# Kernel optimization log

Measured on AMD Instinct MI355X. Metric: run time of the kernel, lower is better.

The kernel has to match this reference:

```python
import jax, jax.numpy as jnp
import numpy as np
import math

B, S, CIN, H, W = 8, 8, 64, 32, 32
COUT, K = 128, 3
PW = COUT * CIN * K * K  # 73728
P = PW + COUT            # 73856


def setup_inputs() -> dict:
    key = jax.random.key(0)
    ks = jax.random.split(key, 6)
    return {
        "x": jax.random.normal(ks[0], (B, S, CIN, H, W), dtype=jnp.float32),
        "e": jax.random.normal(ks[1], (S, P), dtype=jnp.float32),
        "mu_w": jax.random.normal(ks[2], (PW,), dtype=jnp.float32) * 0.02,
        "rho_w": jax.random.normal(ks[3], (PW,), dtype=jnp.float32) * 0.5,
        "mu_b": jax.random.normal(ks[4], (COUT,), dtype=jnp.float32) * 0.02,
        "rho_b": jax.random.normal(ks[5], (COUT,), dtype=jnp.float32) * 0.5,
    }


def _unit_log_mfg(v):
    # v: [s_n, D]; -log(2*pi)*D/2 - sum(v**2)/2  (scalar, matching torch code)
    two_pi = jnp.asarray(2.0 * math.pi, v.dtype)
    return -jnp.log(two_pi) * (v.shape[1] / 2.0) - jnp.sum(v * v) / 2.0


def reference(x, e, mu_w, rho_w, mu_b, rho_b):
    s_n = e.shape[0]
    cout = mu_b.shape[0]
    cin = x.shape[2]
    k = int(round(math.sqrt(mu_w.shape[0] / (cout * cin))))
    pw = mu_w.shape[0]

    sig_w = jax.nn.softplus(rho_w)  # log(1+exp(rho))
    sig_b = jax.nn.softplus(rho_b)
    w = mu_w[None, :] + sig_w[None, :] * e[:, :pw]          # [s_n, PW]
    b = mu_b[None, :] + sig_b[None, :] * e[:, pw:pw + cout]  # [s_n, COUT]

    entropy_q = jnp.sum(jnp.log(sig_w)) + jnp.sum(jnp.log(sig_b))
    cross_entropy_qp = _unit_log_mfg(w) + _unit_log_mfg(b)
    kl_qp = -entropy_q - cross_entropy_qp

    w5 = w.reshape(s_n, cout, cin, k, k)  # per-sample OIHW kernels

    # per-sample conv: vmap over the sample axis j; batch conv over data axis i
    def conv_one(xj, wj):  # xj [B,CIN,H,W], wj [COUT,CIN,K,K]
        return jax.lax.conv(xj, wj, (1, 1), 'VALID')

    out = jax.vmap(conv_one, in_axes=(1, 0), out_axes=1)(x, w5)  # [B,S,COUT,H',W']
    out = out + b[None, :, :, None, None]
    return out, kl_qp
```

## Files before the change

kernel.cpp:

```cpp
#include <hip/hip_runtime.h>
#include <hip/hip_bf16.h>
#include <math.h>

#define Bn    8
#define Sn    8
#define COUTc 128
#define PWc   73728
#define Pc    73856
#define WOc   30
#define NPIX  900
#define GPIX  7200
#define NSTEP 9
#define TILE  128
#define NT2   57
#define NSLOT 129

typedef __bf16 bf16;
typedef bf16  bf16x8 __attribute__((ext_vector_type(8)));
typedef float f32x4v __attribute__((ext_vector_type(4)));
typedef float f32x16 __attribute__((ext_vector_type(16)));

__device__ __forceinline__ float softplus_f(float x) {
    return fmaxf(x, 0.f) + log1pf(expf(-fabsf(x)));
}

__device__ __forceinline__ unsigned int pack2(float a, float b) {
    unsigned short ua = __builtin_bit_cast(unsigned short, (bf16)a);
    unsigned short ub = __builtin_bit_cast(unsigned short, (bf16)b);
    return ((unsigned int)ub << 16) | (unsigned int)ua;
}

__device__ __forceinline__ void gl16(const void* g, void* l) {
    typedef __attribute__((address_space(1))) void gvoid;
    typedef __attribute__((address_space(3))) void lvoid;
    __builtin_amdgcn_global_load_lds((gvoid*)g, (lvoid*)l, 16, 0, 0);
}

__global__ __launch_bounds__(256) void prep_all(
        const float* __restrict__ xg, const float* __restrict__ e,
        const float* __restrict__ mu_w, const float* __restrict__ rho_w,
        const float* __restrict__ mu_b, const float* __restrict__ rho_b,
        bf16* __restrict__ xt, bf16* __restrict__ wimg,
        float* __restrict__ bq, float* __restrict__ slots) {
    const int bid = blockIdx.x;
    const int t   = threadIdx.x;

    if (bid < 512) {
        const int img = bid >> 3;
        const int oct = t & 7;
        const int p0  = ((bid & 7) * 32 + (t >> 3)) * 4;
        const float* src = xg + ((size_t)img << 16) + (size_t)(oct * 8) * 1024 + p0;
        f32x4v v[8];
        #pragma unroll
        for (int j = 0; j < 8; ++j)
            v[j] = *reinterpret_cast<const f32x4v*>(src + (size_t)j * 1024);
        char* dstB = (char*)xt + (((size_t)(img << 10) + p0) << 7) + (oct << 4);
        #pragma unroll
        for (int i = 0; i < 4; ++i) {
            uint4 pk;
            pk.x = pack2(v[0][i], v[1][i]);
            pk.y = pack2(v[2][i], v[3][i]);
            pk.z = pack2(v[4][i], v[5][i]);
            pk.w = pack2(v[6][i], v[7][i]);
            *reinterpret_cast<uint4*>(dstB + (size_t)i * 128) = pk;
        }
        return;
    }

    float ls = 0.f, sq = 0.f;
    if (bid < 640) {
        const int rb    = bid - 512;
        const int sg2   = rb >> 5;
        const int chunk = rb & 31;
        const int gidx  = chunk * 256 + t;
        const int co    = gidx >> 6;
        const int ci    = gidx & 63;
        const int p0    = co * 576 + ci * 9;
        float mu[9], sg[9];
        #pragma unroll
        for (int r = 0; r < 9; ++r) {
            mu[r] = mu_w[p0 + r];
            sg[r] = softplus_f(rho_w[p0 + r]);
        }
        if (sg2 == 0) {
            #pragma unroll
            for (int r = 0; r < 9; ++r) ls += logf(sg[r]);
        }
        const int dstp = (co << 6) + (((ci >> 3) ^ (co & 7)) << 3) + (ci & 7);
        #pragma unroll
        for (int si = 0; si < 2; ++si) {
            const int s = sg2 * 2 + si;
            const float* es = e + s * Pc + p0;
            #pragma unroll
            for (int r = 0; r < 9; ++r) {
                float wv = fmaf(sg[r], es[r], mu[r]);
                wimg[((s * NSTEP + r) << 13) + dstp] = (bf16)wv;
                sq += wv * wv;
            }
        }
    } else {
        if (t < COUTc) {
            float sig = softplus_f(rho_b[t]);
            ls = logf(sig);
            float mu = mu_b[t];
            #pragma unroll
            for (int s = 0; s < Sn; ++s) {
                float bv = fmaf(sig, e[s * Pc + PWc + t], mu);
                bq[s * COUTc + t] = bv;
                sq += bv * bv;
            }
        }
    }

    #pragma unroll
    for (int off = 32; off > 0; off >>= 1) {
        ls += __shfl_down(ls, off);
        sq += __shfl_down(sq, off);
    }
    __shared__ float sls[4], ssq[4];
    const int lane = t & 63, wd = t >> 6;
    if (lane == 0) { sls[wd] = ls; ssq[wd] = sq; }
    __syncthreads();
    if (t == 0) {
        slots[2 * (bid - 512)]     = sls[0] + sls[1] + sls[2] + sls[3];
        slots[2 * (bid - 512) + 1] = ssq[0] + ssq[1] + ssq[2] + ssq[3];
    }
}

__global__ __launch_bounds__(256) void conv_mfma(
        const bf16* __restrict__ xt, const bf16* __restrict__ wimg,
        const float* __restrict__ bq, const float* __restrict__ slots,
        float* __restrict__ out, float* __restrict__ klout) {
    const int bid  = blockIdx.x;
    const int s    = bid & 7;
    const int tile = bid >> 3;
    const int t    = threadIdx.x;
    const int lane = t & 63;
    const int w    = t >> 6;
    const int wr   = w >> 1;
    const int wc   = w & 1;

    __shared__ bf16 Wbuf[2][8192];
    __shared__ bf16 Xbuf[2][8192];

    const char* wsrcL = (const char*)wimg + ((size_t)(s * NSTEP) << 14)
                      + (w << 12) + (lane << 4);

    const char *x0, *x1, *x2, *x3;
    #pragma unroll
    for (int q = 0; q < 4; ++q) {
        int pix = w * 32 + q * 8 + (lane >> 3);
        int g   = tile * TILE + pix;
        if (g >= GPIX) g = GPIX - 1;
        int b2 = g / NPIX;
        int rr = g - b2 * NPIX;
        int oy = rr / WOc;
        int ox = rr - oy * WOc;
        int m  = (lane & 7) ^ (pix & 7);
        const char* ptr = (const char*)xt
            + ((((size_t)(b2 * Sn + s) << 10) + oy * 32 + ox) << 7) + (m << 4);
        if (q == 0) x0 = ptr; else if (q == 1) x1 = ptr;
        else if (q == 2) x2 = ptr; else x3 = ptr;
    }

    f32x16 acc[2][2];
    #pragma unroll
    for (int i = 0; i < 2; ++i)
        #pragma unroll
        for (int j = 0; j < 2; ++j)
            #pragma unroll
            for (int k = 0; k < 16; ++k)
                acc[i][j][k] = 0.f;

    #define STAGE(stepc, b)                                                  \
    {                                                                        \
        const char* ws_ = wsrcL + ((stepc) << 14);                           \
        char* wl_ = (char*)(&Wbuf[(b)][0]) + (w << 12);                      \
        gl16(ws_,        wl_);                                               \
        gl16(ws_ + 1024, wl_ + 1024);                                        \
        gl16(ws_ + 2048, wl_ + 2048);                                        \
        gl16(ws_ + 3072, wl_ + 3072);                                        \
        const int roff_ = (((stepc) / 3) * 32 + ((stepc) % 3)) * 128;        \
        char* xl_ = (char*)(&Xbuf[(b)][0]) + (w << 12);                      \
        gl16(x0 + roff_, xl_);                                               \
        gl16(x1 + roff_, xl_ + 1024);                                        \
        gl16(x2 + roff_, xl_ + 2048);                                        \
        gl16(x3 + roff_, xl_ + 3072);                                        \
    }

    #define COMPUTE(b)                                                       \
    {                                                                        \
        const bf16* Wl_ = &Wbuf[(b)][0];                                     \
        const bf16* Xl_ = &Xbuf[(b)][0];                                     \
        _Pragma("unroll")                                                    \
        for (int kc = 0; kc < 4; ++kc) {                                     \
            const int oct_ = ((kc << 1) + (lane >> 5)) ^ (lane & 7);         \
            bf16x8 af0 = *reinterpret_cast<const bf16x8*>(                   \
                Wl_ + ((wr * 64 + (lane & 31)) << 6) + (oct_ << 3));         \
            bf16x8 af1 = *reinterpret_cast<const bf16x8*>(                   \
                Wl_ + ((wr * 64 + 32 + (lane & 31)) << 6) + (oct_ << 3));    \
            bf16x8 bf0 = *reinterpret_cast<const bf16x8*>(                   \
                Xl_ + ((wc * 64 + (lane & 31)) << 6) + (oct_ << 3));         \
            bf16x8 bf1 = *reinterpret_cast<const bf16x8*>(                   \
                Xl_ + ((wc * 64 + 32 + (lane & 31)) << 6) + (oct_ << 3));    \
            acc[0][0] = __builtin_amdgcn_mfma_f32_32x32x16_bf16(af0, bf0, acc[0][0], 0, 0, 0); \
            acc[0][1] = __builtin_amdgcn_mfma_f32_32x32x16_bf16(af0, bf1, acc[0][1], 0, 0, 0); \
            acc[1][0] = __builtin_amdgcn_mfma_f32_32x32x16_bf16(af1, bf0, acc[1][0], 0, 0, 0); \
            acc[1][1] = __builtin_amdgcn_mfma_f32_32x32x16_bf16(af1, bf1, acc[1][1], 0, 0, 0); \
        }                                                                    \
    }

    STAGE(0, 0);
    STAGE(1, 1);

    #define ITER(tt, b)                                                      \
        asm volatile("s_waitcnt vmcnt(8)" ::: "memory");                     \
        __builtin_amdgcn_s_barrier();                                        \
        __builtin_amdgcn_sched_barrier(0);                                   \
        COMPUTE(b);                                                          \
        __builtin_amdgcn_sched_barrier(0);                                   \
        __builtin_amdgcn_s_barrier();                                        \
        STAGE((tt) + 2, b);

    ITER(0, 0)
    ITER(1, 1)
    ITER(2, 0)
    ITER(3, 1)
    ITER(4, 0)
    ITER(5, 1)
    ITER(6, 0)
    asm volatile("s_waitcnt vmcnt(8)" ::: "memory");
    __builtin_amdgcn_s_barrier();
    __builtin_amdgcn_sched_barrier(0);
    COMPUTE(1);
    asm volatile("s_waitcnt vmcnt(0)" ::: "memory");
    __builtin_amdgcn_s_barrier();
    __builtin_amdgcn_sched_barrier(0);
    COMPUTE(0);

    #undef ITER
    #undef COMPUTE
    #undef STAGE

    const int colp = lane & 31;
    const int hi   = lane >> 5;
    #pragma unroll
    for (int ti = 0; ti < 2; ++ti) {
        float bs[16];
        #pragma unroll
        for (int reg = 0; reg < 16; ++reg) {
            int co = wr * 64 + ti * 32 + (reg & 3) + 8 * (reg >> 2) + 4 * hi;
            bs[reg] = bq[s * COUTc + co];
        }
        #pragma unroll
        for (int tj = 0; tj < 2; ++tj) {
            int gg = tile * TILE + wc * 64 + tj * 32 + colp;
            if (gg >= GPIX) continue;
            int b2 = gg / NPIX;
            int r2 = gg - b2 * NPIX;
            float* ob = out + (size_t)(b2 * Sn + s) * (COUTc * NPIX) + r2;
            #pragma unroll
            for (int reg = 0; reg < 16; ++reg) {
                int co = wr * 64 + ti * 32 + (reg & 3) + 8 * (reg >> 2) + 4 * hi;
                ob[co * NPIX] = acc[ti][tj][reg] + bs[reg];
            }
        }
    }

    if (bid == 0 && w == 0) {
        float ls = 0.f, sq = 0.f;
        for (int i2 = lane; i2 < NSLOT; i2 += 64) {
            ls += slots[2 * i2];
            sq += slots[2 * i2 + 1];
        }
        #pragma unroll
        for (int off = 32; off > 0; off >>= 1) {
            ls += __shfl_down(ls, off);
            sq += __shfl_down(sq, off);
        }
        if (lane == 0)
            *klout = -ls + 0.91893853320467274f * (float)Pc + 0.5f * sq;
    }
}

extern "C" void kernel_launch(void* const* d_in, const int* in_sizes, int n_in,
                              void* d_out, int out_size, void* d_ws, size_t ws_size,
                              hipStream_t stream) {
    const float* x     = (const float*)d_in[0];
    const float* e     = (const float*)d_in[1];
    const float* mu_w  = (const float*)d_in[2];
    const float* rho_w = (const float*)d_in[3];
    const float* mu_b  = (const float*)d_in[4];
    const float* rho_b = (const float*)d_in[5];
    float* out = (float*)d_out;

    bf16*  wimg  = (bf16*)d_ws;
    float* bq    = (float*)((char*)d_ws + 1179648);
    float* slots = (float*)((char*)d_ws + 1183744);
    bf16*  xt    = (bf16*)((char*)d_ws + 1187840);

    prep_all<<<dim3(641), dim3(256), 0, stream>>>(
        x, e, mu_w, rho_w, mu_b, rho_b, xt, wimg, bq, slots);

    conv_mfma<<<dim3(NT2 * Sn), dim3(256), 0, stream>>>(
        xt, wimg, bq, slots, out, out + (out_size - 1));
}
```

Baseline: 30.85 us.

## Halve K-step size in conv MFMA pipeline to 18 half-steps with smaller LDS buffers

Splits each of the 9 filter-tap K-steps (64 channels) into two 32-channel half-steps, giving 18 pipeline stages. The LDS double buffers shrink from 32 KB to 16 KB and each stage issues 4 instead of 8 global-to-LDS loads, with a new XOR swizzle on 4 slots. The aim is to cut LDS use, which may let more blocks share a CU, and to use finer-grained prefetch. In exchange it doubles the barrier count and puts less MFMA work between each sync.

Result: slower. 32.09 us (+4.0%).

```diff
diff --git a/kernel.cpp b/kernel.cpp
--- a/kernel.cpp
+++ b/kernel.cpp
@@ -139,28 +139,39 @@
     const int w    = t >> 6;
     const int wr   = w >> 1;
     const int wc   = w & 1;
-
-    __shared__ bf16 Wbuf[2][8192];
-    __shared__ bf16 Xbuf[2][8192];
-
-    const char* wsrcL = (const char*)wimg + ((size_t)(s * NSTEP) << 14)
-                      + (w << 12) + (lane << 4);
-
-    const char *x0, *x1, *x2, *x3;
+    const int hi   = lane >> 5;
+    const int lo   = lane & 31;
+
+    __shared__ bf16 Wbuf[2][4096];
+    __shared__ bf16 Xbuf[2][4096];
+
+    const int srow  = lane >> 2;
+    const int sslot = lane & 3;
+    const int rb23  = (lane >> 4) & 3;
+
+    const char* wsp[2][2];
+    {
+        const int lowslot = sslot ^ rb23 ^ (srow & 3);
+        const char* base = (const char*)wimg + ((size_t)(s * NSTEP) << 14);
+        #pragma unroll
+        for (int q = 0; q < 2; ++q) {
+            int co = w * 32 + q * 16 + srow;
+            const char* p0 = base + co * 128 + lowslot * 16;
+            wsp[0][q] = p0 + (((lane >> 4) & 1) << 6);
+            wsp[1][q] = p0 + ((1 ^ ((lane >> 4) & 1)) << 6);
+        }
+    }
+
+    const char* xsp[2];
     #pragma unroll
-    for (int q = 0; q < 4; ++q) {
-        int pix = w * 32 + q * 8 + (lane >> 3);
+    for (int q = 0; q < 2; ++q) {
+        int pix = w * 32 + q * 16 + srow;
         int g   = tile * TILE + pix;
         if (g >= GPIX) g = GPIX - 1;
-        int b2 = g / NPIX;
-        int rr = g - b2 * NPIX;
-        int oy = rr / WOc;
-        int ox = rr - oy * WOc;
-        int m  = (lane & 7) ^ (pix & 7);
-        const char* ptr = (const char*)xt
-            + ((((size_t)(b2 * Sn + s) << 10) + oy * 32 + ox) << 7) + (m << 4);
-        if (q == 0) x0 = ptr; else if (q == 1) x1 = ptr;
-        else if (q == 2) x2 = ptr; else x3 = ptr;
+        int b2 = g / NPIX, rr = g - b2 * NPIX, oy = rr / WOc, ox = rr - oy * WOc;
+        xsp[q] = (const char*)xt
+            + ((((size_t)(b2 * Sn + s) << 10) + oy * 32 + ox) << 7)
+            + ((sslot ^ rb23) << 4);
     }
 
     f32x16 acc[2][2];
@@ -174,18 +185,16 @@
 
     #define STAGE(stepc, b)                                                  \
     {                                                                        \
-        const char* ws_ = wsrcL + ((stepc) << 14);                           \
-        char* wl_ = (char*)(&Wbuf[(b)][0]) + (w << 12);                      \
-        gl16(ws_,        wl_);                                               \
-        gl16(ws_ + 1024, wl_ + 1024);                                        \
-        gl16(ws_ + 2048, wl_ + 2048);                                        \
-        gl16(ws_ + 3072, wl_ + 3072);                                        \
-        const int roff_ = (((stepc) / 3) * 32 + ((stepc) % 3)) * 128;        \
-        char* xl_ = (char*)(&Xbuf[(b)][0]) + (w << 12);                      \
-        gl16(x0 + roff_, xl_);                                               \
-        gl16(x1 + roff_, xl_ + 1024);                                        \
-        gl16(x2 + roff_, xl_ + 2048);                                        \
-        gl16(x3 + roff_, xl_ + 3072);                                        \
+        constexpr int r_ = (stepc) >> 1;                                     \
+        constexpr int h_ = (stepc) & 1;                                      \
+        constexpr size_t pg_ = (size_t)r_ << 14;                             \
+        constexpr int ro_ = ((r_ / 3) * 32 + (r_ % 3)) * 128 + h_ * 64;      \
+        char* wl_ = (char*)(&Wbuf[(b)][0]) + (w << 11);                      \
+        char* xl_ = (char*)(&Xbuf[(b)][0]) + (w << 11);                      \
+        gl16(wsp[h_][0] + pg_, wl_);                                         \
+        gl16(wsp[h_][1] + pg_, wl_ + 1024);                                  \
+        gl16(xsp[0] + ro_, xl_);                                             \
+        gl16(xsp[1] + ro_, xl_ + 1024);                                      \
     }
 
     #define COMPUTE(b)                                                       \
@@ -193,16 +202,16 @@
         const bf16* Wl_ = &Wbuf[(b)][0];                                     \
         const bf16* Xl_ = &Xbuf[(b)][0];                                     \
         _Pragma("unroll")                                                    \
-        for (int kc = 0; kc < 4; ++kc) {                                     \
-            const int oct_ = ((kc << 1) + (lane >> 5)) ^ (lane & 7);         \
+        for (int kc = 0; kc < 2; ++kc) {                                     \
+            const int slot_ = (((kc << 1) + hi) ^ ((lo >> 2) & 3)) << 3;     \
             bf16x8 af0 = *reinterpret_cast<const bf16x8*>(                   \
-                Wl_ + ((wr * 64 + (lane & 31)) << 6) + (oct_ << 3));         \
+                Wl_ + ((wr * 64 + lo) << 5) + slot_);                        \
             bf16x8 af1 = *reinterpret_cast<const bf16x8*>(                   \
-                Wl_ + ((wr * 64 + 32 + (lane & 31)) << 6) + (oct_ << 3));    \
+                Wl_ + ((wr * 64 + 32 + lo) << 5) + slot_);                   \
             bf16x8 bf0 = *reinterpret_cast<const bf16x8*>(                   \
-                Xl_ + ((wc * 64 + (lane & 31)) << 6) + (oct_ << 3));         \
+                Xl_ + ((wc * 64 + lo) << 5) + slot_);                        \
             bf16x8 bf1 = *reinterpret_cast<const bf16x8*>(                   \
-                Xl_ + ((wc * 64 + 32 + (lane & 31)) << 6) + (oct_ << 3));    \
+                Xl_ + ((wc * 64 + 32 + lo) << 5) + slot_);                   \
             acc[0][0] = __builtin_amdgcn_mfma_f32_32x32x16_bf16(af0, bf0, acc[0][0], 0, 0, 0); \
             acc[0][1] = __builtin_amdgcn_mfma_f32_32x32x16_bf16(af0, bf1, acc[0][1], 0, 0, 0); \
             acc[1][0] = __builtin_amdgcn_mfma_f32_32x32x16_bf16(af1, bf0, acc[1][0], 0, 0, 0); \
@@ -213,37 +222,32 @@
     STAGE(0, 0);
     STAGE(1, 1);
 
-    #define ITER(tt, b)                                                      \
-        asm volatile("s_waitcnt vmcnt(8)" ::: "memory");                     \
+    #define ITER(tt)                                                         \
+        asm volatile("s_waitcnt vmcnt(4)" ::: "memory");                     \
         __builtin_amdgcn_s_barrier();                                        \
         __builtin_amdgcn_sched_barrier(0);                                   \
-        COMPUTE(b);                                                          \
+        COMPUTE((tt) & 1);                                                   \
         __builtin_amdgcn_sched_barrier(0);                                   \
         __builtin_amdgcn_s_barrier();                                        \
-        STAGE((tt) + 2, b);
-
-    ITER(0, 0)
-    ITER(1, 1)
-    ITER(2, 0)
-    ITER(3, 1)
-    ITER(4, 0)
-    ITER(5, 1)
-    ITER(6, 0)
-    asm volatile("s_waitcnt vmcnt(8)" ::: "memory");
+        STAGE((tt) + 2, (tt) & 1);
+
+    ITER(0)  ITER(1)  ITER(2)  ITER(3)
+    ITER(4)  ITER(5)  ITER(6)  ITER(7)
+    ITER(8)  ITER(9)  ITER(10) ITER(11)
+    ITER(12) ITER(13) ITER(14) ITER(15)
+    asm volatile("s_waitcnt vmcnt(4)" ::: "memory");
+    __builtin_amdgcn_s_barrier();
+    __builtin_amdgcn_sched_barrier(0);
+    COMPUTE(0);
+    asm volatile("s_waitcnt vmcnt(0)" ::: "memory");
     __builtin_amdgcn_s_barrier();
     __builtin_amdgcn_sched_barrier(0);
     COMPUTE(1);
-    asm volatile("s_waitcnt vmcnt(0)" ::: "memory");
-    __builtin_amdgcn_s_barrier();
-    __builtin_amdgcn_sched_barrier(0);
-    COMPUTE(0);
 
     #undef ITER
     #undef COMPUTE
     #undef STAGE
 
-    const int colp = lane & 31;
-    const int hi   = lane >> 5;
     #pragma unroll
     for (int ti = 0; ti < 2; ++ti) {
         float bs[16];
@@ -254,7 +258,7 @@
         }
         #pragma unroll
         for (int tj = 0; tj < 2; ++tj) {
-            int gg = tile * TILE + wc * 64 + tj * 32 + colp;
+            int gg = tile * TILE + wc * 64 + tj * 32 + lo;
             if (gg >= GPIX) continue;
             int b2 = gg / NPIX;
             int r2 = gg - b2 * NPIX;
```
